# Kernel tuning notes

Hardware: AMD Instinct MI355X
Metric: run time of the kernel (lower is better)

Reference implementation:

```python
import jax, jax.numpy as jnp
from jax import lax
import numpy as np

IMG = 1024          # original image H = W
HD = WD = 256       # detection feature map (stride 4)
CD = 128            # detection feature channels
HS = WS = 512       # segmentation feature map (stride 2)
CS = 32             # segmentation feature channels
FC = 1024           # detection head conv / fc filters
K = 2000            # pre-NMS topk
MAX_OUT = 500       # max proposals after NMS
NMS_THR = 1.0       # distance threshold in detection-grid units
CROP = 48           # instance crop size (instance_crop_size // 2)
CI = 64             # instance conv channels


def _conv(x, w, b):
    # x: [H,W,Cin] single map -> same-padded conv
    y = lax.conv_general_dilated(x[None], w, (1, 1), 'SAME',
                                 dimension_numbers=('NHWC', 'HWIO', 'NHWC'))[0]
    return y + b


def _conv_b(x, w, b):
    # x: [N,H,W,Cin] batched conv
    y = lax.conv_general_dilated(x, w, (1, 1), 'SAME',
                                 dimension_numbers=('NHWC', 'HWIO', 'NHWC'))
    return y + b


def setup_inputs() -> dict:
    key = jax.random.key(0)
    ks = jax.random.split(key, 10)
    s = 0.02
    return {
        'detection_features': jax.random.normal(ks[0], (HD, WD, CD), jnp.float32),
        'segmentation_features': jax.random.normal(ks[1], (HS, WS, CS), jnp.float32),
        'Wc': jax.random.normal(ks[2], (3, 3, CD, FC), jnp.float32) * s,
        'bc': jnp.zeros((FC,), jnp.float32),
        'Wfc': jax.random.normal(ks[3], (1, 1, FC, FC), jnp.float32) * s,
        'bfc': jnp.zeros((FC,), jnp.float32),
        'Ws': jax.random.normal(ks[4], (1, 1, FC, 1), jnp.float32) * s,
        'bs': jnp.zeros((1,), jnp.float32),
        'Wr': jax.random.normal(ks[5], (1, 1, FC, 2), jnp.float32) * s,
        'br': jnp.zeros((2,), jnp.float32),
        'Wi': jax.random.normal(ks[6], (3, 3, CS, CI), jnp.float32) * s,
        'bi': jnp.zeros((CI,), jnp.float32),
        'Wo': jax.random.normal(ks[7], (3, 3, CI, 1), jnp.float32) * s,
        'bo': jnp.zeros((1,), jnp.float32),
    }


def _forward(detection_features, segmentation_features,
             Wc, bc, Wfc, bfc, Ws, bs, Wr, br, Wi, bi, Wo, bo):
    x = jax.nn.relu(_conv(detection_features, Wc, bc))
    x = jax.nn.relu(_conv(x, Wfc, bfc))
    scores = jax.nn.sigmoid(_conv(x, Ws, bs))[..., 0]          # [HD,WD]
    reg = _conv(x, Wr, br)                                      # [HD,WD,2] offsets in grid units

    # ---- proposal_locations: decode, topk, distance-threshold NMS ----
    yy, xx = jnp.meshgrid(jnp.arange(HD, dtype=jnp.float32),
                          jnp.arange(WD, dtype=jnp.float32), indexing='ij')
    ctr = jnp.stack([yy, xx], axis=-1) + 0.5                    # cell centers
    locs = (ctr + reg) / jnp.array([HD, WD], jnp.float32)       # normalized [0,1]
    flat_scores = scores.reshape(-1)                            # [HD*WD]
    flat_locs = locs.reshape(-1, 2)

    top_s, top_i = lax.top_k(flat_scores, K)                    # pre-NMS topk (sorted desc)
    cand = flat_locs[top_i]                                     # [K,2] normalized

    grid_xy = cand * jnp.array([HD, WD], jnp.float32)           # grid-unit coords
    d2 = jnp.sum((grid_xy[:, None, :] - grid_xy[None, :, :]) ** 2, axis=-1)  # [K,K]
    close = d2 < (NMS_THR * NMS_THR)
    later = jnp.arange(K)[None, :] > jnp.arange(K)[:, None]

    def nms_body(i, suppressed):
        keep_i = jnp.logical_not(suppressed[i])
        return suppressed | (keep_i & close[i] & later[i])

    suppressed = lax.fori_loop(0, K, nms_body, jnp.zeros((K,), jnp.bool_))
    masked = jnp.where(suppressed, -1.0, top_s)
    proposed_scores, sel = lax.top_k(masked, MAX_OUT)           # [500]
    sel_norm = cand[sel]                                        # [500,2]
    decoded = sel_norm * jnp.float32(IMG)                       # pixel coords

    # ---- instance head: crop stride-2 seg features around each proposal ----
    seg_loc = decoded / 2.0
    start = jnp.clip(jnp.round(seg_loc - CROP / 2), 0, HS - CROP).astype(jnp.int32)  # [500,2]

    def crop_one(st):
        return lax.dynamic_slice(segmentation_features, (st[0], st[1], 0), (CROP, CROP, CS))

    crops = jax.vmap(crop_one)(start)                           # [500,48,48,CS]
    h = jax.nn.relu(_conv_b(crops, Wi, bi))                     # [500,48,48,CI]
    instance_output = jax.nn.sigmoid(_conv_b(h, Wo, bo))        # [500,48,48,1]

    cy, cx = jnp.meshgrid(jnp.arange(CROP), jnp.arange(CROP), indexing='ij')
    instance_coords = start[:, None, None, :] + jnp.stack([cy, cx], axis=-1)[None]  # [500,48,48,2]

    return proposed_scores, decoded, instance_output, instance_coords


def reference(detection_features, segmentation_features,
              Wc, bc, Wfc, bfc, Ws, bs, Wr, br, Wi, bi, Wo, bo):
    return _forward(detection_features, segmentation_features,
                    Wc, bc, Wfc, bfc, Ws, bs, Wr, br, Wi, bi, Wo, bo)
```

## Files before the change

### kernel.cpp

```cpp
#include <hip/hip_runtime.h>
#include <math.h>

#define KTOP 2000
#define MAXOUT 500
#define CANDCAP 4096
#define NSEL 3600
#define RCC 32
#define RC2 16

typedef __attribute__((ext_vector_type(8))) short short8;
typedef __attribute__((ext_vector_type(4))) float f32x4;
typedef __attribute__((ext_vector_type(4))) double f64x4;

__device__ __forceinline__ unsigned short f2bf(float f) {
  unsigned int u = __float_as_uint(f);
  unsigned int r = ((u >> 16) & 1u) + 0x7FFFu;
  return (unsigned short)((u + r) >> 16);
}

__device__ __forceinline__ void ld_lds16(const void* g, void* l) {
  __builtin_amdgcn_global_load_lds((const unsigned int*)g, (unsigned int*)l,
                                   16, 0, 0);
}

__device__ __forceinline__ void hard_barrier() {
  asm volatile("" ::: "memory");
  __builtin_amdgcn_sched_barrier(0);
  __builtin_amdgcn_s_barrier();
  __builtin_amdgcn_sched_barrier(0);
  asm volatile("" ::: "memory");
}

__global__ __launch_bounds__(256) void transpose_bf16_kernel(
    const float* __restrict__ W, unsigned short* __restrict__ WT, int K, int N)
{
  __shared__ float t[32][33];
  const int k0 = blockIdx.x << 5, n0 = blockIdx.y << 5;
  const int tid = threadIdx.x;
  const int r = tid >> 5, c = tid & 31;
#pragma unroll
  for (int p = 0; p < 4; ++p)
    t[r + (p << 3)][c] = W[(size_t)(k0 + r + (p << 3)) * N + n0 + c];
  __syncthreads();
#pragma unroll
  for (int p = 0; p < 4; ++p)
    WT[(size_t)(n0 + r + (p << 3)) * K + k0 + c] = f2bf(t[c][r + (p << 3)]);
}

__global__ __launch_bounds__(256) void prep_wib_kernel(
    const float* __restrict__ Wi, unsigned short* __restrict__ WiB)
{
  const int t = blockIdx.x * 256 + threadIdx.x;
  if (t < 9 * 64 * 32) {
    const int tap = t / 2048, r = t & 2047, co = r >> 5, ci = r & 31;
    WiB[t] = f2bf(Wi[((size_t)tap * 32 + ci) * 64 + co]);
  }
}

__global__ __launch_bounds__(256) void pad_df_bf16(
    const float* __restrict__ df, unsigned short* __restrict__ dfb)
{
  const int t = blockIdx.x * 256 + threadIdx.x;
  if (t >= 258 * 258 * 16) return;
  const int p = t >> 4;
  const int c8 = (t & 15) << 3;
  const int gy = p / 258 - 1, gx = p % 258 - 1;
  uint4 out = make_uint4(0, 0, 0, 0);
  if (gy >= 0 && gy < 256 && gx >= 0 && gx < 256) {
    const float* src = &df[((size_t)(gy * 256 + gx)) * 128 + c8];
    const float4 v0 = *(const float4*)src;
    const float4 v1 = *(const float4*)(src + 4);
    out.x = (unsigned int)f2bf(v0.x) | ((unsigned int)f2bf(v0.y) << 16);
    out.y = (unsigned int)f2bf(v0.z) | ((unsigned int)f2bf(v0.w) << 16);
    out.z = (unsigned int)f2bf(v1.x) | ((unsigned int)f2bf(v1.y) << 16);
    out.w = (unsigned int)f2bf(v1.z) | ((unsigned int)f2bf(v1.w) << 16);
  }
  *(uint4*)&dfb[(size_t)p * 128 + c8] = out;
}

template <typename IssueFn>
__device__ __forceinline__ void ktile_phases(
    const unsigned short* __restrict__ A0, const unsigned short* __restrict__ B0,
    const int arow, const int brow, const int ok0, const int ok1,
    f32x4 (&acc)[8][4], IssueFn&& iss, const bool do_issue)
{
  short8 Af[4][2], Bf[2][2][2];
#pragma unroll
  for (int m = 0; m < 4; ++m) {
    Af[m][0] = *(const short8*)&A0[((arow + (m << 4)) << 6) + ok0];
    Af[m][1] = *(const short8*)&A0[((arow + (m << 4)) << 6) + ok1];
  }
#pragma unroll
  for (int n = 0; n < 2; ++n) {
    Bf[0][n][0] = *(const short8*)&B0[((brow + (n << 4)) << 6) + ok0];
    Bf[0][n][1] = *(const short8*)&B0[((brow + (n << 4)) << 6) + ok1];
  }
  hard_barrier();
  __builtin_amdgcn_s_setprio(1);
#pragma unroll
  for (int m = 0; m < 4; ++m)
#pragma unroll
    for (int n = 0; n < 2; ++n) {
      acc[m][n] = __builtin_amdgcn_mfma_f32_16x16x32_bf16(Af[m][0], Bf[0][n][0], acc[m][n], 0, 0, 0);
      acc[m][n] = __builtin_amdgcn_mfma_f32_16x16x32_bf16(Af[m][1], Bf[0][n][1], acc[m][n], 0, 0, 0);
    }
  __builtin_amdgcn_s_setprio(0);
  hard_barrier();
#pragma unroll
  for (int n = 0; n < 2; ++n) {
    Bf[1][n][0] = *(const short8*)&B0[((brow + ((n + 2) << 4)) << 6) + ok0];
    Bf[1][n][1] = *(const short8*)&B0[((brow + ((n + 2) << 4)) << 6) + ok1];
  }
  hard_barrier();
  __builtin_amdgcn_s_setprio(1);
#pragma unroll
  for (int m = 0; m < 4; ++m)
#pragma unroll
    for (int n = 0; n < 2; ++n) {
      acc[m][n + 2] = __builtin_amdgcn_mfma_f32_16x16x32_bf16(Af[m][0], Bf[1][n][0], acc[m][n + 2], 0, 0, 0);
      acc[m][n + 2] = __builtin_amdgcn_mfma_f32_16x16x32_bf16(Af[m][1], Bf[1][n][1], acc[m][n + 2], 0, 0, 0);
    }
  __builtin_amdgcn_s_setprio(0);
  hard_barrier();
#pragma unroll
  for (int m = 0; m < 4; ++m) {
    Af[m][0] = *(const short8*)&A0[((arow + 64 + (m << 4)) << 6) + ok0];
    Af[m][1] = *(const short8*)&A0[((arow + 64 + (m << 4)) << 6) + ok1];
  }
  hard_barrier();
  __builtin_amdgcn_s_setprio(1);
#pragma unroll
  for (int m = 0; m < 4; ++m)
#pragma unroll
    for (int n = 0; n < 2; ++n) {
      acc[m + 4][n + 2] = __builtin_amdgcn_mfma_f32_16x16x32_bf16(Af[m][0], Bf[1][n][0], acc[m + 4][n + 2], 0, 0, 0);
      acc[m + 4][n + 2] = __builtin_amdgcn_mfma_f32_16x16x32_bf16(Af[m][1], Bf[1][n][1], acc[m + 4][n + 2], 0, 0, 0);
    }
  __builtin_amdgcn_s_setprio(0);
  hard_barrier();
  if (do_issue) iss();
  __builtin_amdgcn_s_setprio(1);
#pragma unroll
  for (int m = 0; m < 4; ++m)
#pragma unroll
    for (int n = 0; n < 2; ++n) {
      acc[m + 4][n] = __builtin_amdgcn_mfma_f32_16x16x32_bf16(Af[m][0], Bf[0][n][0], acc[m + 4][n], 0, 0, 0);
      acc[m + 4][n] = __builtin_amdgcn_mfma_f32_16x16x32_bf16(Af[m][1], Bf[0][n][1], acc[m + 4][n], 0, 0, 0);
    }
  __builtin_amdgcn_s_setprio(0);
  hard_barrier();
}

__global__ __launch_bounds__(512) void conv1_mfma(
    const unsigned short* __restrict__ dfb, const unsigned short* __restrict__ WcT,
    const float* __restrict__ bc, unsigned short* __restrict__ x1b, int pt0)
{
  __shared__ __align__(16) unsigned short smem[65536];
  const int tid = threadIdx.x;
  const int wv = tid >> 6, lane = tid & 63;
  const int wr = wv >> 2, wc = wv & 3;
  const int l15 = lane & 15, quad = lane >> 4;
  const int n0 = blockIdx.x << 8;
  const int lm0 = blockIdx.y << 8;
  const int Pbase = (pt0 << 6) + lm0;
  const int y = Pbase >> 8;
  const int tr = tid >> 3, g8 = tid & 7;
  const int xg = ((g8 ^ (tr & 7)) << 4);
  const int axr = l15 & 7;
  const int ok0 = ((quad ^ axr) << 3);
  const int ok1 = (((4 + quad) ^ axr) << 3);
  const int arow = (wr << 7) + l15;
  const int brow = (wc << 6) + l15;

  float bcv[4];
#pragma unroll
  for (int j = 0; j < 4; ++j) bcv[j] = bc[n0 + (wc << 6) + (j << 4) + l15];

  f32x4 acc[8][4];
  const f32x4 z4 = {0.f, 0.f, 0.f, 0.f};
#pragma unroll
  for (int i = 0; i < 8; ++i)
#pragma unroll
    for (int j = 0; j < 4; ++j) acc[i][j] = z4;

  const char* WB = (const char*)WcT + ((size_t)(n0 + tr) * 1152) * 2 + xg;
  unsigned short* lA = &smem[(tr << 6) + (g8 << 3)];

  auto issue = [&](int kt, int buf) {
    const int tap = kt >> 1, ci0 = (kt & 1) << 6;
    const int dy = tap / 3 - 1, dx = tap % 3 - 1;
    const char* Ab = (const char*)dfb +
        (((size_t)((y + dy + 1) * 258 + dx + 1)) * 128 + ci0) * 2 +
        (size_t)tr * 256 + xg;
    unsigned short* la = lA + buf * 32768;
    unsigned short* lb = la + 16384;
    const char* Bb = WB + (size_t)kt * 128;
#pragma unroll
    for (int i = 0; i < 4; ++i)
      ld_lds16(Ab + (size_t)i * 16384, la + i * 4096);
#pragma unroll
    for (int i = 0; i < 4; ++i)
      ld_lds16(Bb + (size_t)i * 147456, lb + i * 4096);
  };

  issue(0, 0);
  issue(1, 1);
#pragma unroll 2
  for (int kt = 0; kt < 18; ++kt) {
    const int buf = kt & 1;
    if (kt < 17) asm volatile("s_waitcnt vmcnt(8)" ::: "memory");
    else         asm volatile("s_waitcnt vmcnt(0)" ::: "memory");
    hard_barrier();
    ktile_phases(&smem[buf * 32768], &smem[buf * 32768 + 16384],
                 arow, brow, ok0, ok1, acc,
                 [&]() { issue(kt + 2, buf); }, kt < 16);
  }

#pragma unroll
  for (int m = 0; m < 8; ++m)
#pragma unroll
    for (int n = 0; n < 4; ++n) {
      const int col = n0 + (wc << 6) + (n << 4) + l15;
      const float bb = bcv[n];
#pragma unroll
      for (int rg = 0; rg < 4; ++rg) {
        const int row = lm0 + (wr << 7) + (m << 4) + (quad << 2) + rg;
        const float v = fmaxf(acc[m][n][rg] + bb, 0.f);
        x1b[(size_t)row * 1024 + col] = f2bf(v);
      }
    }
}

__global__ __launch_bounds__(512) void fc_mfma(
    const unsigned short* __restrict__ x1b, const unsigned short* __restrict__ WfcT,
    const float* __restrict__ bfc, const float* __restrict__ Wsc,
    float* __restrict__ part, int pt0)
{
  __shared__ __align__(16) unsigned short smem[65536];
  const int tid = threadIdx.x;
  const int wv = tid >> 6, lane = tid & 63;
  const int wr = wv >> 2, wc = wv & 3;
  const int l15 = lane & 15, quad = lane >> 4;
  const int n0 = blockIdx.x << 8;
  const int lm0 = blockIdx.y << 8;
  const int Pbase = (pt0 << 6) + lm0;
  const int tr = tid >> 3, g8 = tid & 7;
  const int xg = ((g8 ^ (tr & 7)) << 4);
  const int axr = l15 & 7;
  const int ok0 = ((quad ^ axr) << 3);
  const int ok1 = (((4 + quad) ^ axr) << 3);
  const int arow = (wr << 7) + l15;
  const int brow = (wc << 6) + l15;

  float wsv[4], bfv[4];
#pragma unroll
  for (int j = 0; j < 4; ++j) {
    const int col = n0 + (wc << 6) + (j << 4) + l15;
    wsv[j] = Wsc[col];
    bfv[j] = bfc[col];
  }

  f32x4 acc[8][4];
  const f32x4 z4 = {0.f, 0.f, 0.f, 0.f};
#pragma unroll
  for (int i = 0; i < 8; ++i)
#pragma unroll
    for (int j = 0; j < 4; ++j) acc[i][j] = z4;

  const char* AB = (const char*)x1b + ((size_t)(lm0 + tr) * 1024) * 2 + xg;
  const char* WB = (const char*)WfcT + ((size_t)(n0 + tr) * 1024) * 2 + xg;
  unsigned short* lA = &smem[(tr << 6) + (g8 << 3)];

  auto issue = [&](int kt, int buf) {
    unsigned short* la = lA + buf * 32768;
    unsigned short* lb = la + 16384;
    const char* Ab = AB + (size_t)kt * 128;
    const char* Bb = WB + (size_t)kt * 128;
#pragma unroll
    for (int i = 0; i < 4; ++i)
      ld_lds16(Ab + (size_t)i * 131072, la + i * 4096);
#pragma unroll
    for (int i = 0; i < 4; ++i)
      ld_lds16(Bb + (size_t)i * 131072, lb + i * 4096);
  };

  issue(0, 0);
  issue(1, 1);
#pragma unroll 2
  for (int kt = 0; kt < 16; ++kt) {
    const int buf = kt & 1;
    if (kt < 15) asm volatile("s_waitcnt vmcnt(8)" ::: "memory");
    else         asm volatile("s_waitcnt vmcnt(0)" ::: "memory");
    hard_barrier();
    ktile_phases(&smem[buf * 32768], &smem[buf * 32768 + 16384],
                 arow, brow, ok0, ok1, acc,
                 [&]() { issue(kt + 2, buf); }, kt < 14);
  }

  float* red = (float*)smem;
#pragma unroll
  for (int m = 0; m < 8; ++m)
#pragma unroll
    for (int rg = 0; rg < 4; ++rg) {
      float ps = 0.f;
#pragma unroll
      for (int n = 0; n < 4; ++n) {
        const float v = fmaxf(acc[m][n][rg] + bfv[n], 0.f);
        ps = fmaf(v, wsv[n], ps);
      }
#pragma unroll
      for (int off = 1; off <= 8; off <<= 1)
        ps += __shfl_xor(ps, off, 64);
      if (l15 == 0) {
        const int row = (wr << 7) + (m << 4) + (quad << 2) + rg;
        red[row * 5 + wc] = ps;
      }
    }
  __syncthreads();
  if (tid < 256) {
    float s = 0.f;
#pragma unroll
    for (int w8 = 0; w8 < 4; ++w8) s += red[tid * 5 + w8];
    part[(size_t)blockIdx.x * 65536 + Pbase + tid] = s;
  }
}

__global__ __launch_bounds__(256) void head_finalize_kernel(
    const float* __restrict__ part, const float* __restrict__ bs,
    float* __restrict__ scores)
{
  const int pix = blockIdx.x * 256 + threadIdx.x;
  float s = 0.f;
#pragma unroll
  for (int cb = 0; cb < 4; ++cb) s += part[(size_t)cb * 65536 + pix];
  s += bs[0];
  scores[pix] = 1.f / (1.f + expf(-s));
}

__global__ __launch_bounds__(1024) void select_kernel(
    const float* __restrict__ scores, unsigned int* __restrict__ cand_idx,
    unsigned int* __restrict__ cand_cnt)
{
  __shared__ unsigned int hist[256];
  __shared__ unsigned int sh_prefix, sh_sub;
  __shared__ int scan_s[1024];
  const int tid = threadIdx.x;

  unsigned int prefix = 0u;
  int need = NSEL;
  for (int byte = 3; byte >= 0; --byte) {
    if (tid < 256) hist[tid] = 0u;
    __syncthreads();
    const int sh = byte * 8;
    const unsigned int mhi = (byte == 3) ? 0u : (0xFFFFFFFFu << (sh + 8));
    for (int i = tid; i < 65536; i += 1024) {
      const unsigned int b = __float_as_uint(scores[i]);
      if ((b & mhi) == prefix) atomicAdd(&hist[(b >> sh) & 255u], 1u);
    }
    __syncthreads();
    for (int off = 1; off < 256; off <<= 1) {
      unsigned int add = 0u;
      if (tid < 256 && tid + off < 256) add = hist[tid + off];
      __syncthreads();
      if (tid < 256) hist[tid] += add;
      __syncthreads();
    }
    if (tid < 256) {
      const unsigned int sv = hist[tid];
      const unsigned int above = (tid == 255) ? 0u : hist[tid + 1];
      if ((int)above < need && (int)sv >= need) {
        sh_prefix = prefix | ((unsigned)tid << sh);
        sh_sub = above;
      }
    }
    __syncthreads();
    prefix = sh_prefix;
    need -= (int)sh_sub;
    __syncthreads();
  }
  const float thr = __uint_as_float(prefix);

  const int b0 = tid << 6;
  int my = 0;
  for (int k = 0; k < 64; ++k)
    if (scores[b0 + k] >= thr) ++my;
  scan_s[tid] = my;
  __syncthreads();
  for (int off = 1; off < 1024; off <<= 1) {
    const int a = scan_s[tid];
    const int b = (tid >= off) ? scan_s[tid - off] : 0;
    __syncthreads();
    scan_s[tid] = a + b;
    __syncthreads();
  }
  int pos = scan_s[tid] - my;
  const int total = scan_s[1023];
  for (int k = 0; k < 64; ++k) {
    if (scores[b0 + k] >= thr) {
      if (pos < CANDCAP) cand_idx[pos] = (unsigned int)(b0 + k);
      ++pos;
    }
  }
  if (tid == 0)
    *cand_cnt = (unsigned int)(total > CANDCAP ? CANDCAP : total);
}

#define PSTR 133
__global__ __launch_bounds__(512) void rescore_conv(
    const float* __restrict__ df, const float* __restrict__ Wc,
    const float* __restrict__ bc,
    const unsigned int* __restrict__ cand_idx,
    const unsigned int* __restrict__ cand_cnt,
    double* __restrict__ x1g)
{
  __shared__ double patt[2][RCC * PSTR];
  __shared__ int rrs[RCC], ccs[RCC];
  const int cnt = (int)*cand_cnt;
  const int nb = blockIdx.x & 1;
  const int c0 = (blockIdx.x >> 1) * RCC;
  if (c0 >= cnt) return;
  const int tid = threadIdx.x;
  const int wv = tid >> 6, lane = tid & 63;
  const int m = lane & 15, quad = lane >> 4;
  const int co_base = (nb << 9) + (wv << 6);

  if (tid < RCC) {
    const int slot = (c0 + tid < cnt) ? c0 + tid : c0;
    const unsigned int idx = cand_idx[slot];
    rrs[tid] = (int)(idx >> 8); ccs[tid] = (int)(idx & 255u);
  }
  __syncthreads();

  float sv[8];
  auto ldregs = [&](int tap) {
    const int dy = tap / 3 - 1, dx = tap % 3 - 1;
#pragma unroll
    for (int j = 0; j < 8; ++j) {
      const int p = tid + (j << 9);
      const int c = p >> 7, ci = p & 127;
      const int gy = rrs[c] + dy, gx = ccs[c] + dx;
      float v = 0.f;
      if (gy >= 0 && gy < 256 && gx >= 0 && gx < 256)
        v = df[((size_t)((gy << 8) + gx)) * 128 + ci];
      sv[j] = v;
    }
  };
  auto wrlds = [&](int b) {
#pragma unroll
    for (int j = 0; j < 8; ++j) {
      const int p = tid + (j << 9);
      const int c = p >> 7, ci = p & 127;
      patt[b][c * PSTR + ci] = (double)sv[j];
    }
  };

  f64x4 acc[2][4];
  const f64x4 z4 = {0.0, 0.0, 0.0, 0.0};
#pragma unroll
  for (int ct = 0; ct < 2; ++ct)
#pragma unroll
    for (int t = 0; t < 4; ++t) acc[ct][t] = z4;

  ldregs(0);
  wrlds(0);
  __syncthreads();
  int buf = 0;
  for (int tap = 0; tap < 9; ++tap) {
    if (tap < 8) ldregs(tap + 1);
    const float* wrow = &Wc[(size_t)(tap * 128 + quad) * 1024 + co_base + m];
    float wf[4], wn[4];
#pragma unroll
    for (int t = 0; t < 4; ++t) wf[t] = wrow[t << 4];
#pragma unroll
    for (int t = 0; t < 4; ++t) wn[t] = wrow[(size_t)4096 + (t << 4)];
    for (int k4 = 0; k4 < 32; ++k4) {
      float w2[4];
      if (k4 + 2 < 32) {
#pragma unroll
        for (int t = 0; t < 4; ++t)
          w2[t] = wrow[(size_t)((k4 + 2) << 2) * 1024 + (t << 4)];
      }
      const double a0 = patt[buf][m * PSTR + (k4 << 2) + quad];
      const double a1 = patt[buf][(16 + m) * PSTR + (k4 << 2) + quad];
#pragma unroll
      for (int t = 0; t < 4; ++t)
        acc[0][t] = __builtin_amdgcn_mfma_f64_16x16x4f64(a0, (double)wf[t], acc[0][t], 0, 0, 0);
#pragma unroll
      for (int t = 0; t < 4; ++t)
        acc[1][t] = __builtin_amdgcn_mfma_f64_16x16x4f64(a1, (double)wf[t], acc[1][t], 0, 0, 0);
      if (k4 + 1 < 32) {
#pragma unroll
        for (int t = 0; t < 4; ++t) wf[t] = wn[t];
      }
      if (k4 + 2 < 32) {
#pragma unroll
        for (int t = 0; t < 4; ++t) wn[t] = w2[t];
      }
    }
    if (tap < 8) wrlds(buf ^ 1);
    __syncthreads();
    buf ^= 1;
  }
#pragma unroll
  for (int ct = 0; ct < 2; ++ct)
#pragma unroll
    for (int t = 0; t < 4; ++t) {
      const int co = co_base + (t << 4) + m;
      const double bb = (double)bc[co];
#pragma unroll
      for (int rg = 0; rg < 4; ++rg) {
        const int cand = (ct << 4) + (quad << 2) + rg;
        if (c0 + cand < cnt) {
          const double v = acc[ct][t][rg] + bb;
          x1g[(size_t)(c0 + cand) * 1024 + co] = v > 0.0 ? v : 0.0;
        }
      }
    }
}

__global__ __launch_bounds__(512) void rescore_fc(
    const double* __restrict__ x1g, const float* __restrict__ Wfc,
    const float* __restrict__ bfc, const float* __restrict__ Wsc,
    const float* __restrict__ bs, const float* __restrict__ Wrg,
    const float* __restrict__ br,
    const unsigned int* __restrict__ cand_cnt,
    unsigned long long* __restrict__ cand_sb,
    double* __restrict__ cand_ry, double* __restrict__ cand_rx)
{
  __shared__ double xbuf[2][16 * PSTR];
  __shared__ double partw[3][8][16];
  const int cnt = (int)*cand_cnt;
  const int c0 = blockIdx.x * RC2;
  if (c0 >= cnt) return;
  const int tid = threadIdx.x;
  const int wv = tid >> 6, lane = tid & 63;
  const int m = lane & 15, quad = lane >> 4;
  const int co_base = wv << 7;

  double sx[4];
  auto ldregs = [&](int kc) {
#pragma unroll
    for (int j = 0; j < 4; ++j) {
      const int p = tid + (j << 9);
      const int c = p >> 7, k = p & 127;
      const int row = (c0 + c < cnt) ? c0 + c : c0;
      sx[j] = x1g[(size_t)row * 1024 + (kc << 7) + k];
    }
  };
  auto wrlds = [&](int b) {
#pragma unroll
    for (int j = 0; j < 4; ++j) {
      const int p = tid + (j << 9);
      const int c = p >> 7, k = p & 127;
      xbuf[b][c * PSTR + k] = sx[j];
    }
  };

  f64x4 acc[8];
  const f64x4 z4 = {0.0, 0.0, 0.0, 0.0};
#pragma unroll
  for (int t = 0; t < 8; ++t) acc[t] = z4;

  ldregs(0);
  wrlds(0);
  __syncthreads();
  int buf = 0;
  for (int kc = 0; kc < 8; ++kc) {
    if (kc < 7) ldregs(kc + 1);
    const float* wrow = &Wfc[(size_t)((kc << 7) + quad) * 1024 + co_base + m];
    float wf[8];
#pragma unroll
    for (int t = 0; t < 8; ++t) wf[t] = wrow[t << 4];
    for (int k4 = 0; k4 < 32; ++k4) {
      float wn[8];
      if (k4 + 1 < 32) {
#pragma unroll
        for (int t = 0; t < 8; ++t)
          wn[t] = wrow[(size_t)((k4 + 1) << 2) * 1024 + (t << 4)];
      }
      const double a = xbuf[buf][m * PSTR + (k4 << 2) + quad];
#pragma unroll
      for (int t = 0; t < 8; ++t)
        acc[t] = __builtin_amdgcn_mfma_f64_16x16x4f64(a, (double)wf[t], acc[t], 0, 0, 0);
      if (k4 + 1 < 32) {
#pragma unroll
        for (int t = 0; t < 8; ++t) wf[t] = wn[t];
      }
    }
    if (kc < 7) wrlds(buf ^ 1);
    __syncthreads();
    buf ^= 1;
  }

  double ps[4] = {0, 0, 0, 0}, py[4] = {0, 0, 0, 0}, px[4] = {0, 0, 0, 0};
#pragma unroll
  for (int t = 0; t < 8; ++t) {
    const int co = co_base + (t << 4) + m;
    const double bfv = (double)bfc[co];
    const double wsv = (double)Wsc[co];
    const double w0 = (double)Wrg[co * 2], w1 = (double)Wrg[co * 2 + 1];
#pragma unroll
    for (int rg = 0; rg < 4; ++rg) {
      double v = acc[t][rg] + bfv;
      v = v > 0.0 ? v : 0.0;
      ps[rg] = fma(v, wsv, ps[rg]);
      py[rg] = fma(v, w0, py[rg]);
      px[rg] = fma(v, w1, px[rg]);
    }
  }
#pragma unroll
  for (int off = 1; off <= 8; off <<= 1) {
#pragma unroll
    for (int rg = 0; rg < 4; ++rg) {
      ps[rg] += __shfl_xor(ps[rg], off, 64);
      py[rg] += __shfl_xor(py[rg], off, 64);
      px[rg] += __shfl_xor(px[rg], off, 64);
    }
  }
  if (m == 0) {
#pragma unroll
    for (int rg = 0; rg < 4; ++rg) {
      const int cand = (quad << 2) + rg;
      partw[0][wv][cand] = ps[rg];
      partw[1][wv][cand] = py[rg];
      partw[2][wv][cand] = px[rg];
    }
  }
  __syncthreads();
  if (tid < 48) {
    const int cand = tid & 15, h = tid >> 4;
    double s = 0.0;
#pragma unroll
    for (int w8 = 0; w8 < 8; ++w8) s += partw[h][w8][cand];
    if (c0 + cand < cnt) {
      if (h == 0) {
        const double lg = s + (double)bs[0];
        const double sg = 1.0 / (1.0 + exp(-lg));
        cand_sb[c0 + cand] = (unsigned long long)__double_as_longlong(sg);
      } else if (h == 1) cand_ry[c0 + cand] = s + (double)br[0];
      else               cand_rx[c0 + cand] = s + (double)br[1];
    }
  }
}

#define PROP_LDS 102400
__global__ __launch_bounds__(1024) void proposal_kernel(
    const unsigned int* __restrict__ cand_idx,
    const unsigned int* __restrict__ cand_cnt,
    const unsigned long long* __restrict__ cand_sb,
    const double* __restrict__ cand_ry, const double* __restrict__ cand_rx,
    unsigned int* __restrict__ cellrank,
    double* __restrict__ cyg, double* __restrict__ cxg,
    int* __restrict__ startb, float* __restrict__ out_ps,
    float* __restrict__ out_dec)
{
  extern __shared__ __align__(16) char dynsm[];
  unsigned long long* sk = (unsigned long long*)dynsm;
  unsigned int* si = (unsigned int*)(dynsm + 16384);
  int* scan = (int*)(dynsm + 24576);
  unsigned short* nbrs = (unsigned short*)(dynsm + 32768);
  unsigned char* kept = (unsigned char*)(dynsm + 98304);
  unsigned char* nbrc = (unsigned char*)(dynsm + 100352);

  __shared__ unsigned int hist[256];
  __shared__ unsigned long long sh_pref;
  __shared__ unsigned int sh_sub;
  __shared__ volatile unsigned int changed;
  __shared__ int sh_maxreg;

  const int tid = threadIdx.x;
  const int cnt = (int)*cand_cnt;

  for (int i = tid; i < 65536; i += 1024) cellrank[i] = 0xFFFFFFFFu;

  unsigned long long prefix = 0ull;
  int need = KTOP;
  for (int byte = 7; byte >= 0; --byte) {
    if (tid < 256) hist[tid] = 0u;
    __syncthreads();
    const int sh = byte * 8;
    const unsigned long long mhi =
        (byte == 7) ? 0ull : (0xFFFFFFFFFFFFFFFFull << (sh + 8));
    for (int i = tid; i < cnt; i += 1024) {
      const unsigned long long k = cand_sb[i];
      if ((k & mhi) == prefix) atomicAdd(&hist[(unsigned int)((k >> sh) & 255u)], 1u);
    }
    __syncthreads();
    for (int off = 1; off < 256; off <<= 1) {
      unsigned int add = 0u;
      if (tid < 256 && tid + off < 256) add = hist[tid + off];
      __syncthreads();
      if (tid < 256) hist[tid] += add;
      __syncthreads();
    }
    if (tid < 256) {
      const unsigned int sv = hist[tid];
      const unsigned int above = (tid == 255) ? 0u : hist[tid + 1];
      if ((int)above < need && (int)sv >= need) {
        sh_pref = prefix | ((unsigned long long)(unsigned)tid << sh);
        sh_sub = above;
      }
    }
    __syncthreads();
    prefix = sh_pref;
    need -= (int)sh_sub;
    __syncthreads();
  }
  const unsigned long long T = prefix;

  const int s0 = tid << 2;
  unsigned long long kv[4];
  int ca = 0, cb = 0;
#pragma unroll
  for (int q = 0; q < 4; ++q) {
    const int s = s0 + q;
    kv[q] = (s < cnt) ? cand_sb[s] : 0ull;
    if (s < cnt) { if (kv[q] > T) ++ca; else if (kv[q] == T) ++cb; }
  }
  scan[tid] = ca;
  __syncthreads();
  for (int off = 1; off < 1024; off <<= 1) {
    const int a = scan[tid];
    const int b = (tid >= off) ? scan[tid - off] : 0;
    __syncthreads();
    scan[tid] = a + b;
    __syncthreads();
  }
  int posA = scan[tid] - ca;
  const int atot = scan[1023];
  __syncthreads();
  scan[tid] = cb;
  __syncthreads();
  for (int off = 1; off < 1024; off <<= 1) {
    const int a = scan[tid];
    const int b = (tid >= off) ? scan[tid - off] : 0;
    __syncthreads();
    scan[tid] = a + b;
    __syncthreads();
  }
  int posB = atot + (scan[tid] - cb);
  __syncthreads();
#pragma unroll
  for (int q = 0; q < 4; ++q) {
    const int s = s0 + q;
    if (s < cnt) {
      if (kv[q] > T) {
        sk[posA] = kv[q]; si[posA] = (unsigned int)s; ++posA;
      } else if (kv[q] == T) {
        if (posB < KTOP) { sk[posB] = kv[q]; si[posB] = (unsigned int)s; }
        ++posB;
      }
    }
  }
  __syncthreads();
  for (int i = tid; i < 2048; i += 1024)
    if (i >= KTOP) { sk[i] = 0ull; si[i] = 0u; }
  if (tid == 0) sh_maxreg = 0;
  __syncthreads();

  for (int k = 2; k <= 2048; k <<= 1) {
    for (int j = k >> 1; j > 0; j >>= 1) {
      const int i = (tid & (j - 1)) | ((tid & ~(j - 1)) << 1);
      const int ixj = i | j;
      const unsigned long long a = sk[i], b = sk[ixj];
      const unsigned int ia = si[i], ib = si[ixj];
      const bool up = ((i & k) == 0);
      const bool lt = (a < b) || (a == b && ia > ib);
      const bool gt = (a > b) || (a == b && ia < ib);
      if (up ? lt : gt) {
        sk[i] = b; sk[ixj] = a;
        si[i] = ib; si[ixj] = ia;
      }
      __syncthreads();
    }
  }

  for (int r = tid; r < KTOP; r += 1024) {
    const unsigned int slot = si[r];
    const unsigned int idx = cand_idx[slot];
    const int row = (int)(idx >> 8), col = (int)(idx & 255u);
    const double ry = cand_ry[slot], rx = cand_rx[slot];
    cyg[r] = ((double)row + 0.5) + ry;
    cxg[r] = ((double)col + 0.5) + rx;
    kept[r] = 1; nbrc[r] = 0;
    cellrank[idx] = (unsigned int)r;
    atomicMax(&sh_maxreg, __float_as_int((float)fabs(ry)));
    atomicMax(&sh_maxreg, __float_as_int((float)fabs(rx)));
  }
  __syncthreads();
  const float maxreg = __int_as_float(sh_maxreg);
  int rad = (int)(1.0f + 2.0f * maxreg) + 1;
  if (rad > 8) rad = 8;
  if (rad < 1) rad = 1;

  for (int r = tid; r < KTOP; r += 1024) {
    const unsigned int idx = cand_idx[si[r]];
    const int row = (int)(idx >> 8), col = (int)(idx & 255u);
    int n = 0;
    const double pyr = cyg[r], pxr = cxg[r];
    for (int dy = -rad; dy <= rad; ++dy) {
      const int yy = row + dy; if (yy < 0 || yy >= 256) continue;
      for (int dx = -rad; dx <= rad; ++dx) {
        if (dy == 0 && dx == 0) continue;
        const int xx = col + dx; if (xx < 0 || xx >= 256) continue;
        const unsigned int q = cellrank[yy * 256 + xx];
        if (q < (unsigned int)r) {
          const double t1 = __dsub_rn(pyr, cyg[q]);
          const double t2 = __dsub_rn(pxr, cxg[q]);
          const double d2 = __dadd_rn(__dmul_rn(t1, t1), __dmul_rn(t2, t2));
          if (d2 < 1.0) { if (n < 16) nbrs[(r << 4) + n] = (unsigned short)q; ++n; }
        }
      }
    }
    nbrc[r] = (unsigned char)(n < 16 ? n : 16);
  }
  __syncthreads();

  for (int it = 0; it < 4096; ++it) {
    __syncthreads();
    if (tid == 0) changed = 0;
    __syncthreads();
    for (int r = tid; r < KTOP; r += 1024) {
      const int nc = nbrc[r];
      if (nc) {
        int kvv = 1;
        for (int t = 0; t < nc; ++t)
          if (kept[nbrs[(r << 4) + t]]) { kvv = 0; break; }
        if (kvv != (int)kept[r]) { kept[r] = (unsigned char)kvv; changed = 1; }
      }
    }
    __syncthreads();
    if (changed == 0) break;
  }

  scan[tid]        = (tid < KTOP) ? (int)kept[tid] : 0;
  scan[tid + 1024] = (tid + 1024 < KTOP) ? (int)kept[tid + 1024] : 0;
  __syncthreads();
  for (int off = 1; off < 2048; off <<= 1) {
    const int a0 = scan[tid];
    const int b0 = (tid >= off) ? scan[tid - off] : 0;
    const int a1 = scan[tid + 1024];
    const int b1 = (tid + 1024 >= off) ? scan[tid + 1024 - off] : 0;
    __syncthreads();
    scan[tid] = a0 + b0;
    scan[tid + 1024] = a1 + b1;
    __syncthreads();
  }
  const int total = scan[KTOP - 1];

  for (int r = tid; r < KTOP; r += 1024) {
    int slot = -1;
    if (kept[r]) { const int p = scan[r] - 1; if (p < MAXOUT) slot = p; }
    else { const int p = total + (r - scan[r]); if (p < MAXOUT) slot = p; }
    if (slot >= 0) {
      const double sg = __longlong_as_double((long long)sk[r]);
      out_ps[slot] = kept[r] ? (float)sg : -1.0f;
      const double py = cyg[r], px = cxg[r];
      out_dec[slot * 2]     = (float)(py * 4.0);
      out_dec[slot * 2 + 1] = (float)(px * 4.0);
      int sy = (int)rint(py * 2.0 - 24.0);
      int sx = (int)rint(px * 2.0 - 24.0);
      sy = sy < 0 ? 0 : (sy > 464 ? 464 : sy);
      sx = sx < 0 ? 0 : (sx > 464 ? 464 : sx);
      startb[slot * 2] = sy; startb[slot * 2 + 1] = sx;
    }
  }
}

#define ISTR 40
__global__ __launch_bounds__(256) void conv_i_mfma(
    const float* __restrict__ seg, const unsigned short* __restrict__ WiB,
    const float* __restrict__ bi, const int* __restrict__ startb,
    unsigned short* __restrict__ h, int inst0)
{
  __shared__ __align__(16) unsigned short ins[500 * ISTR];
  const int li = blockIdx.y;
  const int inst = inst0 + li;
  const int tile = blockIdx.x;
  const int r0 = tile << 3;
  const int tid = threadIdx.x;
  const int sy = startb[inst * 2], sx = startb[inst * 2 + 1];

  for (int p = tid; p < 500; p += 256) {
    const int rr = p / 50, cc2 = p - rr * 50;
    const int ir = r0 - 1 + rr, ic = cc2 - 1;
    unsigned short* dst = &ins[p * ISTR];
    if (ir >= 0 && ir < 48 && ic >= 0 && ic < 48) {
      const float* src = &seg[((size_t)(sy + ir) * 512 + (sx + ic)) * 32];
#pragma unroll
      for (int q = 0; q < 8; ++q) {
        const float4 v = *(const float4*)&src[q << 2];
        const unsigned int lo = (unsigned int)f2bf(v.x) | ((unsigned int)f2bf(v.y) << 16);
        const unsigned int hi = (unsigned int)f2bf(v.z) | ((unsigned int)f2bf(v.w) << 16);
        *(uint2*)&dst[q << 2] = make_uint2(lo, hi);
      }
    } else {
#pragma unroll
      for (int q = 0; q < 4; ++q) *(uint4*)&dst[q << 3] = make_uint4(0, 0, 0, 0);
    }
  }
  __syncthreads();

  const int wv = tid >> 6, lane = tid & 63;
  const int l15 = lane & 15, quad = lane >> 4;
  const int wmb = wv * 96;

  int pbase[6];
#pragma unroll
  for (int i = 0; i < 6; ++i) {
    const int m = wmb + (i << 4) + l15;
    pbase[i] = (m / 48 + 1) * 50 + (m % 48) + 1;
  }

  f32x4 acc[6][4];
  const f32x4 z4 = {0.f, 0.f, 0.f, 0.f};
#pragma unroll
  for (int i = 0; i < 6; ++i)
#pragma unroll
    for (int j = 0; j < 4; ++j) acc[i][j] = z4;

  for (int tap = 0; tap < 9; ++tap) {
    const int off = (tap / 3 - 1) * 50 + (tap % 3 - 1);
    short8 b[4];
#pragma unroll
    for (int j = 0; j < 4; ++j)
      b[j] = *(const short8*)&WiB[((tap << 6) + (j << 4) + l15) * 32 + (quad << 3)];
#pragma unroll
    for (int i = 0; i < 6; ++i) {
      const short8 a = *(const short8*)&ins[(pbase[i] + off) * ISTR + (quad << 3)];
#pragma unroll
      for (int j = 0; j < 4; ++j)
        acc[i][j] = __builtin_amdgcn_mfma_f32_16x16x32_bf16(a, b[j], acc[i][j], 0, 0, 0);
    }
  }

  float bv[4];
#pragma unroll
  for (int j = 0; j < 4; ++j) bv[j] = bi[(j << 4) + l15];

  for (int half = 0; half < 2; ++half) {
    __syncthreads();
    if ((wv >> 1) == half) {
#pragma unroll
      for (int i = 0; i < 6; ++i)
#pragma unroll
        for (int j = 0; j < 4; ++j)
#pragma unroll
          for (int rg = 0; rg < 4; ++rg) {
            const int m = wmb + (i << 4) + (quad << 2) + rg;
            const int pp = m - half * 192;
            const float v = fmaxf(acc[i][j][rg] + bv[j], 0.f);
            ins[pp * 72 + (j << 4) + l15] = f2bf(v);
          }
    }
    __syncthreads();
    for (int t = tid; t < 192 * 8; t += 256) {
      const int pp = t >> 3, c8 = t & 7;
      const uint4 v = *(const uint4*)&ins[pp * 72 + (c8 << 3)];
      *(uint4*)&h[((size_t)li * 2304 + (tile * 384 + half * 192 + pp)) * 64 + (c8 << 3)] = v;
    }
  }
}

__global__ __launch_bounds__(256) void conv_o_kernel(
    const unsigned short* __restrict__ h, const float* __restrict__ Wo,
    const float* __restrict__ bo, const int* __restrict__ startb,
    float* __restrict__ out_io, float* __restrict__ out_ic, int inst0)
{
  __shared__ __align__(16) unsigned short hs[324 * 72];
  __shared__ float wos[576];
  const int li = blockIdx.y;
  const int inst = inst0 + li;
  const int tile = blockIdx.x;
  const int ty0 = (tile / 3) << 4;
  const int tx0 = (tile % 3) << 4;
  const int tid = threadIdx.x;

  for (int i = tid; i < 576; i += 256) wos[i] = Wo[i];
  for (int p = tid; p < 324; p += 256) {
    const int iy = p / 18, ix = p - iy * 18;
    const int gy = ty0 - 1 + iy, gx = tx0 - 1 + ix;
    unsigned short* dst = &hs[p * 72];
    if (gy >= 0 && gy < 48 && gx >= 0 && gx < 48) {
      const unsigned short* src = &h[((size_t)li * 2304 + gy * 48 + gx) * 64];
#pragma unroll
      for (int q = 0; q < 8; ++q) *(uint4*)&dst[q << 3] = *(const uint4*)&src[q << 3];
    } else {
#pragma unroll
      for (int q = 0; q < 8; ++q) *(uint4*)&dst[q << 3] = make_uint4(0, 0, 0, 0);
    }
  }
  __syncthreads();

  const int ly = tid >> 4, lx = tid & 15;
  float a = 0.f;
#pragma unroll
  for (int ky = 0; ky < 3; ++ky)
#pragma unroll
    for (int kx = 0; kx < 3; ++kx) {
      const unsigned short* hp = &hs[((ly + ky) * 18 + lx + kx) * 72];
      const float* wp = &wos[(ky * 3 + kx) << 6];
#pragma unroll
      for (int c8 = 0; c8 < 8; ++c8) {
        const uint4 hv = *(const uint4*)&hp[c8 << 3];
        const unsigned int uu[4] = {hv.x, hv.y, hv.z, hv.w};
#pragma unroll
        for (int e = 0; e < 4; ++e) {
          const float f0 = __uint_as_float(uu[e] << 16);
          const float f1 = __uint_as_float(uu[e] & 0xFFFF0000u);
          a = fmaf(f0, wp[(c8 << 3) + (e << 1)], a);
          a = fmaf(f1, wp[(c8 << 3) + (e << 1) + 1], a);
        }
      }
    }
  a += bo[0];
  const float o = 1.f / (1.f + expf(-a));
  const int gy = ty0 + ly, gx = tx0 + lx;
  const size_t p = ((size_t)inst * 48 + gy) * 48 + gx;
  out_io[p] = o;
  const int sy = startb[inst * 2], sx = startb[inst * 2 + 1];
  out_ic[p * 2]     = (float)(sy + gy);
  out_ic[p * 2 + 1] = (float)(sx + gx);
}

extern "C" void kernel_launch(void* const* d_in, const int* in_sizes, int n_in,
                              void* d_out, int out_size, void* d_ws, size_t ws_size,
                              hipStream_t stream)
{
  const float* df  = (const float*)d_in[0];
  const float* seg = (const float*)d_in[1];
  const float* Wc  = (const float*)d_in[2];
  const float* bc  = (const float*)d_in[3];
  const float* Wfc = (const float*)d_in[4];
  const float* bfc = (const float*)d_in[5];
  const float* Wsc = (const float*)d_in[6];
  const float* bs  = (const float*)d_in[7];
  const float* Wrg = (const float*)d_in[8];
  const float* br  = (const float*)d_in[9];
  const float* Wi  = (const float*)d_in[10];
  const float* bi  = (const float*)d_in[11];
  const float* Wo  = (const float*)d_in[12];
  const float* bo  = (const float*)d_in[13];

  const size_t SZ_WCT = 2359296ull, SZ_WFT = 2097152ull, SZ_WIB = 36864ull,
               SZ_DFB = 17040384ull,
               SZ_PART = 2097152ull, SZ_SC = 262144ull, SZ_CR = 262144ull,
               SZ_STB = 4096ull, SZ_CI = CANDCAP * 4ull,
               SZ_SB = CANDCAP * 8ull, SZ_RY = CANDCAP * 8ull,
               SZ_RX = CANDCAP * 8ull, SZ_CY = 16384ull, SZ_CX = 16384ull,
               SZ_X1G = (size_t)CANDCAP * 1024ull * 8ull,
               SZ_CNT = 256ull;
  const size_t FIXED = SZ_WCT + SZ_WFT + SZ_WIB + SZ_DFB + SZ_PART + SZ_SC +
                       SZ_CR + SZ_STB + SZ_CI + SZ_SB + SZ_RY + SZ_RX +
                       SZ_CY + SZ_CX + SZ_X1G + SZ_CNT;
  char* w = (char*)d_ws;
  size_t region = (ws_size > FIXED) ? ((ws_size - FIXED) & ~(size_t)255) : 0;
  char* fb = w + region;
  unsigned short* WcT = (unsigned short*)fb;   fb += SZ_WCT;
  unsigned short* WfcT = (unsigned short*)fb;  fb += SZ_WFT;
  unsigned short* WiB = (unsigned short*)fb;   fb += SZ_WIB;
  unsigned short* dfb = (unsigned short*)fb;   fb += SZ_DFB;
  float* part = (float*)fb;                    fb += SZ_PART;
  float* scores = (float*)fb;                  fb += SZ_SC;
  unsigned int* cellrank = (unsigned int*)fb;  fb += SZ_CR;
  int* startb = (int*)fb;                      fb += SZ_STB;
  unsigned int* cand_idx = (unsigned int*)fb;  fb += SZ_CI;
  unsigned long long* cand_sb = (unsigned long long*)fb; fb += SZ_SB;
  double* cand_ry = (double*)fb;               fb += SZ_RY;
  double* cand_rx = (double*)fb;               fb += SZ_RX;
  double* cyg = (double*)fb;                   fb += SZ_CY;
  double* cxg = (double*)fb;                   fb += SZ_CX;
  double* x1g = (double*)fb;                   fb += SZ_X1G;
  unsigned int* cand_cnt = (unsigned int*)fb;
  unsigned short* x1b = (unsigned short*)w;
  unsigned short* hb = (unsigned short*)w;

  size_t tiles_fit = region / 131072ull;
  int pt_chunk = 4;
  while ((size_t)(pt_chunk * 2) <= tiles_fit && pt_chunk < 1024) pt_chunk <<= 1;
  size_t inst_fit = region / 294912ull;
  const int opts[12] = {500, 250, 125, 100, 50, 25, 20, 10, 5, 4, 2, 1};
  int inst_chunk = 1;
  for (int o = 0; o < 12; ++o)
    if ((size_t)opts[o] <= inst_fit) { inst_chunk = opts[o]; break; }

  float* out = (float*)d_out;
  float* out_ps  = out;
  float* out_dec = out + 500;
  float* out_io  = out + 1500;
  float* out_ic  = out + 1153500;

  transpose_bf16_kernel<<<dim3(36, 32), 256, 0, stream>>>(Wc, WcT, 1152, 1024);
  transpose_bf16_kernel<<<dim3(32, 32), 256, 0, stream>>>(Wfc, WfcT, 1024, 1024);
  prep_wib_kernel<<<72, 256, 0, stream>>>(Wi, WiB);
  pad_df_bf16<<<4161, 256, 0, stream>>>(df, dfb);

  for (int c = 0; c < 1024 / pt_chunk; ++c) {
    conv1_mfma<<<dim3(4, pt_chunk / 4), 512, 0, stream>>>(dfb, WcT, bc, x1b,
                                                          c * pt_chunk);
    fc_mfma<<<dim3(4, pt_chunk / 4), 512, 0, stream>>>(x1b, WfcT, bfc, Wsc,
                                                       part, c * pt_chunk);
  }
  head_finalize_kernel<<<256, 256, 0, stream>>>(part, bs, scores);
  select_kernel<<<1, 1024, 0, stream>>>(scores, cand_idx, cand_cnt);
  rescore_conv<<<(CANDCAP / RCC) * 2, 512, 0, stream>>>(df, Wc, bc, cand_idx,
                                                        cand_cnt, x1g);
  rescore_fc<<<CANDCAP / RC2, 512, 0, stream>>>(x1g, Wfc, bfc, Wsc, bs, Wrg,
                                                br, cand_cnt, cand_sb,
                                                cand_ry, cand_rx);
  proposal_kernel<<<1, 1024, PROP_LDS, stream>>>(cand_idx, cand_cnt, cand_sb,
                                                 cand_ry, cand_rx, cellrank,
                                                 cyg, cxg, startb, out_ps,
                                                 out_dec);
  for (int c = 0; c < 500 / inst_chunk; ++c) {
    conv_i_mfma<<<dim3(6, inst_chunk), 256, 0, stream>>>(seg, WiB, bi, startb,
                                                         hb, c * inst_chunk);
    conv_o_kernel<<<dim3(9, inst_chunk), 256, 0, stream>>>(hb, Wo, bo, startb,
                                                           out_io, out_ic,
                                                           c * inst_chunk);
  }
}
```

Baseline: 1.124 ms.

## Pre-convert seg features to bf16 and split rescore conv across more blocks

Adds a pass that converts the full segmentation feature map to bf16 once, so each instance crop load in conv_i_mfma copies bf16 directly instead of converting fp32 per overlapping crop. This reduces redundant global reads and conversion work, since the 500 crops overlap heavily, but adds a 16 MB intermediate buffer and an extra full-map pass. Separately, rescore_conv now splits output channels four ways instead of two. Each wave handles one 16-candidate tile instead of two, doubling the block count to raise parallelism at the cost of reloading the candidate patches more often.

```diff
diff --git a/kernel.cpp b/kernel.cpp
--- a/kernel.cpp
+++ b/kernel.cpp
@@ -76,6 +76,22 @@
     out.w = (unsigned int)f2bf(v1.z) | ((unsigned int)f2bf(v1.w) << 16);
   }
   *(uint4*)&dfb[(size_t)p * 128 + c8] = out;
+}
+
+__global__ __launch_bounds__(256) void conv_seg_bf16(
+    const float* __restrict__ seg, unsigned short* __restrict__ segb)
+{
+  const int t = blockIdx.x * 256 + threadIdx.x;
+  if (t >= 512 * 512 * 4) return;
+  const float* src = &seg[(size_t)t * 8];
+  const float4 v0 = *(const float4*)src;
+  const float4 v1 = *(const float4*)(src + 4);
+  uint4 out;
+  out.x = (unsigned int)f2bf(v0.x) | ((unsigned int)f2bf(v0.y) << 16);
+  out.y = (unsigned int)f2bf(v0.z) | ((unsigned int)f2bf(v0.w) << 16);
+  out.z = (unsigned int)f2bf(v1.x) | ((unsigned int)f2bf(v1.y) << 16);
+  out.w = (unsigned int)f2bf(v1.z) | ((unsigned int)f2bf(v1.w) << 16);
+  *(uint4*)&segb[(size_t)t * 8] = out;
 }
 
 template <typename IssueFn>
@@ -416,13 +432,15 @@
   __shared__ double patt[2][RCC * PSTR];
   __shared__ int rrs[RCC], ccs[RCC];
   const int cnt = (int)*cand_cnt;
-  const int nb = blockIdx.x & 1;
-  const int c0 = (blockIdx.x >> 1) * RCC;
+  const int nb = blockIdx.x & 3;
+  const int c0 = (blockIdx.x >> 2) * RCC;
   if (c0 >= cnt) return;
   const int tid = threadIdx.x;
   const int wv = tid >> 6, lane = tid & 63;
   const int m = lane & 15, quad = lane >> 4;
-  const int co_base = (nb << 9) + (wv << 6);
+  const int cg = wv >> 2;
+  const int co_base = (nb << 8) + ((wv & 3) << 6);
+  const int arow = (cg << 4) + m;
 
   if (tid < RCC) {
     const int slot = (c0 + tid < cnt) ? c0 + tid : c0;
@@ -454,12 +472,10 @@
     }
   };
 
-  f64x4 acc[2][4];
+  f64x4 acc[4];
   const f64x4 z4 = {0.0, 0.0, 0.0, 0.0};
 #pragma unroll
-  for (int ct = 0; ct < 2; ++ct)
-#pragma unroll
-    for (int t = 0; t < 4; ++t) acc[ct][t] = z4;
+  for (int t = 0; t < 4; ++t) acc[t] = z4;
 
   ldregs(0);
   wrlds(0);
@@ -480,14 +496,10 @@
         for (int t = 0; t < 4; ++t)
           w2[t] = wrow[(size_t)((k4 + 2) << 2) * 1024 + (t << 4)];
       }
-      const double a0 = patt[buf][m * PSTR + (k4 << 2) + quad];
-      const double a1 = patt[buf][(16 + m) * PSTR + (k4 << 2) + quad];
+      const double a = patt[buf][arow * PSTR + (k4 << 2) + quad];
 #pragma unroll
       for (int t = 0; t < 4; ++t)
-        acc[0][t] = __builtin_amdgcn_mfma_f64_16x16x4f64(a0, (double)wf[t], acc[0][t], 0, 0, 0);
-#pragma unroll
-      for (int t = 0; t < 4; ++t)
-        acc[1][t] = __builtin_amdgcn_mfma_f64_16x16x4f64(a1, (double)wf[t], acc[1][t], 0, 0, 0);
+        acc[t] = __builtin_amdgcn_mfma_f64_16x16x4f64(a, (double)wf[t], acc[t], 0, 0, 0);
       if (k4 + 1 < 32) {
 #pragma unroll
         for (int t = 0; t < 4; ++t) wf[t] = wn[t];
@@ -502,20 +514,18 @@
     buf ^= 1;
   }
 #pragma unroll
-  for (int ct = 0; ct < 2; ++ct)
-#pragma unroll
-    for (int t = 0; t < 4; ++t) {
-      const int co = co_base + (t << 4) + m;
-      const double bb = (double)bc[co];
-#pragma unroll
-      for (int rg = 0; rg < 4; ++rg) {
-        const int cand = (ct << 4) + (quad << 2) + rg;
-        if (c0 + cand < cnt) {
-          const double v = acc[ct][t][rg] + bb;
-          x1g[(size_t)(c0 + cand) * 1024 + co] = v > 0.0 ? v : 0.0;
-        }
-      }
-    }
+  for (int t = 0; t < 4; ++t) {
+    const int co = co_base + (t << 4) + m;
+    const double bb = (double)bc[co];
+#pragma unroll
+    for (int rg = 0; rg < 4; ++rg) {
+      const int cand = (cg << 4) + (quad << 2) + rg;
+      if (c0 + cand < cnt) {
+        const double v = acc[t][rg] + bb;
+        x1g[(size_t)(c0 + cand) * 1024 + co] = v > 0.0 ? v : 0.0;
+      }
+    }
+  }
 }
 
 __global__ __launch_bounds__(512) void rescore_fc(
@@ -869,7 +879,7 @@
 
 #define ISTR 40
 __global__ __launch_bounds__(256) void conv_i_mfma(
-    const float* __restrict__ seg, const unsigned short* __restrict__ WiB,
+    const unsigned short* __restrict__ segb, const unsigned short* __restrict__ WiB,
     const float* __restrict__ bi, const int* __restrict__ startb,
     unsigned short* __restrict__ h, int inst0)
 {
@@ -886,14 +896,10 @@
     const int ir = r0 - 1 + rr, ic = cc2 - 1;
     unsigned short* dst = &ins[p * ISTR];
     if (ir >= 0 && ir < 48 && ic >= 0 && ic < 48) {
-      const float* src = &seg[((size_t)(sy + ir) * 512 + (sx + ic)) * 32];
-#pragma unroll
-      for (int q = 0; q < 8; ++q) {
-        const float4 v = *(const float4*)&src[q << 2];
-        const unsigned int lo = (unsigned int)f2bf(v.x) | ((unsigned int)f2bf(v.y) << 16);
-        const unsigned int hi = (unsigned int)f2bf(v.z) | ((unsigned int)f2bf(v.w) << 16);
-        *(uint2*)&dst[q << 2] = make_uint2(lo, hi);
-      }
+      const unsigned short* src = &segb[((size_t)(sy + ir) * 512 + (sx + ic)) * 32];
+#pragma unroll
+      for (int q = 0; q < 4; ++q)
+        *(uint4*)&dst[q << 3] = *(const uint4*)&src[q << 3];
     } else {
 #pragma unroll
       for (int q = 0; q < 4; ++q) *(uint4*)&dst[q << 3] = make_uint4(0, 0, 0, 0);
@@ -1044,14 +1050,15 @@
 
   const size_t SZ_WCT = 2359296ull, SZ_WFT = 2097152ull, SZ_WIB = 36864ull,
                SZ_DFB = 17040384ull,
+               SZ_SEGB = 16777216ull,
                SZ_PART = 2097152ull, SZ_SC = 262144ull, SZ_CR = 262144ull,
                SZ_STB = 4096ull, SZ_CI = CANDCAP * 4ull,
                SZ_SB = CANDCAP * 8ull, SZ_RY = CANDCAP * 8ull,
                SZ_RX = CANDCAP * 8ull, SZ_CY = 16384ull, SZ_CX = 16384ull,
                SZ_X1G = (size_t)CANDCAP * 1024ull * 8ull,
                SZ_CNT = 256ull;
-  const size_t FIXED = SZ_WCT + SZ_WFT + SZ_WIB + SZ_DFB + SZ_PART + SZ_SC +
-                       SZ_CR + SZ_STB + SZ_CI + SZ_SB + SZ_RY + SZ_RX +
+  const size_t FIXED = SZ_WCT + SZ_WFT + SZ_WIB + SZ_DFB + SZ_SEGB + SZ_PART +
+                       SZ_SC + SZ_CR + SZ_STB + SZ_CI + SZ_SB + SZ_RY + SZ_RX +
                        SZ_CY + SZ_CX + SZ_X1G + SZ_CNT;
   char* w = (char*)d_ws;
   size_t region = (ws_size > FIXED) ? ((ws_size - FIXED) & ~(size_t)255) : 0;
@@ -1060,6 +1067,7 @@
   unsigned short* WfcT = (unsigned short*)fb;  fb += SZ_WFT;
   unsigned short* WiB = (unsigned short*)fb;   fb += SZ_WIB;
   unsigned short* dfb = (unsigned short*)fb;   fb += SZ_DFB;
+  unsigned short* segb = (unsigned short*)fb;  fb += SZ_SEGB;
   float* part = (float*)fb;                    fb += SZ_PART;
   float* scores = (float*)fb;                  fb += SZ_SC;
   unsigned int* cellrank = (unsigned int*)fb;  fb += SZ_CR;
@@ -1094,6 +1102,7 @@
   transpose_bf16_kernel<<<dim3(32, 32), 256, 0, stream>>>(Wfc, WfcT, 1024, 1024);
   prep_wib_kernel<<<72, 256, 0, stream>>>(Wi, WiB);
   pad_df_bf16<<<4161, 256, 0, stream>>>(df, dfb);
+  conv_seg_bf16<<<4096, 256, 0, stream>>>(seg, segb);
 
   for (int c = 0; c < 1024 / pt_chunk; ++c) {
     conv1_mfma<<<dim3(4, pt_chunk / 4), 512, 0, stream>>>(dfb, WcT, bc, x1b,
@@ -1103,7 +1112,7 @@
   }
   head_finalize_kernel<<<256, 256, 0, stream>>>(part, bs, scores);
   select_kernel<<<1, 1024, 0, stream>>>(scores, cand_idx, cand_cnt);
-  rescore_conv<<<(CANDCAP / RCC) * 2, 512, 0, stream>>>(df, Wc, bc, cand_idx,
+  rescore_conv<<<(CANDCAP / RCC) * 4, 512, 0, stream>>>(df, Wc, bc, cand_idx,
                                                         cand_cnt, x1g);
   rescore_fc<<<CANDCAP / RC2, 512, 0, stream>>>(x1g, Wfc, bfc, Wsc, bs, Wrg,
                                                 br, cand_cnt, cand_sb,
@@ -1113,7 +1122,7 @@
                                                  cyg, cxg, startb, out_ps,
                                                  out_dec);
   for (int c = 0; c < 500 / inst_chunk; ++c) {
-    conv_i_mfma<<<dim3(6, inst_chunk), 256, 0, stream>>>(seg, WiB, bi, startb,
+    conv_i_mfma<<<dim3(6, inst_chunk), 256, 0, stream>>>(segb, WiB, bi, startb,
                                                          hb, c * inst_chunk);
     conv_o_kernel<<<dim3(9, inst_chunk), 256, 0, stream>>>(hb, Wo, bo, startb,
                                                            out_io, out_ic,
```

After: 1.132 ms. Within noise of the previous version (+0.7%).
